# Kernel tuning notes

Hardware: AMD Instinct MI355X
Metric: run time of the kernel (lower is better)

The kernel has to match this reference:

```python
import jax, jax.numpy as jnp
import numpy as np

ND, NG, E = 25000, 20000, 1_000_000
DIN_D, DIN_G, H, OUT = 128, 128, 128, 128


def setup_inputs() -> dict:
    key = jax.random.key(0)
    ks = jax.random.split(key, 12)

    def w(k, i, o):
        return jax.random.normal(k, (i, o), jnp.float32) / np.float32(np.sqrt(i))

    return {
        "x_disease": jax.random.normal(ks[0], (ND, DIN_D), jnp.float32),
        "x_gene": jax.random.normal(ks[1], (NG, DIN_G), jnp.float32),
        "src": jax.random.randint(ks[2], (E,), 0, ND, dtype=jnp.int32),  # disease endpoint
        "dst": jax.random.randint(ks[3], (E,), 0, NG, dtype=jnp.int32),  # gene endpoint
        # layer 1, relation disease->gene: lin_l acts on aggregated disease feats, lin_r on gene feats
        "w1_dg_l": w(ks[4], DIN_D, H), "b1_dg": jnp.zeros((H,), jnp.float32), "w1_dg_r": w(ks[5], DIN_G, H),
        # layer 1, relation gene->disease (reverse edges)
        "w1_gd_l": w(ks[6], DIN_G, H), "b1_gd": jnp.zeros((H,), jnp.float32), "w1_gd_r": w(ks[7], DIN_D, H),
        # layer 2
        "w2_dg_l": w(ks[8], H, OUT), "b2_dg": jnp.zeros((OUT,), jnp.float32), "w2_dg_r": w(ks[9], H, OUT),
        "w2_gd_l": w(ks[10], H, OUT), "b2_gd": jnp.zeros((OUT,), jnp.float32), "w2_gd_r": w(ks[11], H, OUT),
    }


def _sage(x_src, x_dst, e_src, e_dst, n_dst, W_l, b_l, W_r):
    """Bipartite SAGEConv: lin_l(mean of source neighbors) + lin_r(x_dst)."""
    msg = x_src[e_src]                                         # [E, d] gather
    s = jax.ops.segment_sum(msg, e_dst, num_segments=n_dst)    # [n_dst, d]
    cnt = jax.ops.segment_sum(jnp.ones((e_dst.shape[0],), x_src.dtype),
                              e_dst, num_segments=n_dst)
    mean = s / jnp.maximum(cnt, 1.0)[:, None]                  # isolated nodes -> 0
    return mean @ W_l + b_l + x_dst @ W_r


def reference(x_disease, x_gene, src, dst,
              w1_dg_l, b1_dg, w1_dg_r, w1_gd_l, b1_gd, w1_gd_r,
              w2_dg_l, b2_dg, w2_dg_r, w2_gd_l, b2_gd, w2_gd_r):
    # HeteroConv aggr='sum': each node type receives from exactly one relation here,
    # so the cross-relation sum is the single relation output.
    g1 = _sage(x_disease, x_gene, src, dst, NG, w1_dg_l, b1_dg, w1_dg_r)   # gene <- disease
    d1 = _sage(x_gene, x_disease, dst, src, ND, w1_gd_l, b1_gd, w1_gd_r)   # disease <- gene (rev)
    g2 = _sage(d1, g1, src, dst, NG, w2_dg_l, b2_dg, w2_dg_r)
    d2 = _sage(g1, d1, dst, src, ND, w2_gd_l, b2_gd, w2_gd_r)
    return d2, g2
```

## Files before the change

kernel.cpp:

```cpp
#include <hip/hip_runtime.h>
#include <hip/hip_fp16.h>

#define ND 25000
#define NG 20000
#define NTOT (ND + NG)
#define NBLK 128
#define PREPB 1024
#define NSB 176
#define DRNG 6250
#define GRNG 5000
#define AGG_SLOTS 1563
#define AGG_GRID (8 * AGG_SLOTS)

typedef _Float16 half8 __attribute__((ext_vector_type(8)));
typedef float f32x4 __attribute__((ext_vector_type(4)));
typedef float f32x2 __attribute__((ext_vector_type(2)));

#define OFF_CNT    0ull
#define OFF_ROW    180224ull
#define OFF_PARTD  360704ull
#define OFF_PARTG  6760704ull
#define OFF_COL    11880704ull
#define OFF_WSW    15880704ull
#define OFF_XDH    16142848ull
#define OFF_XGH    22542848ull
#define OFF_X8D    27662848ull
#define OFF_X8G    30862848ull
#define OFF_MDH    33422848ull
#define OFF_MGH    39822848ull
#define OFF_D1H    44942848ull
#define OFF_G1H    51342848ull
#define OFF_D18    56462848ull
#define OFF_G18    59662848ull

struct WPtrs { const float* w[8]; };

__global__ __launch_bounds__(256) void prep_hist(const float* __restrict__ xd,
                                                 const float* __restrict__ xg,
                                                 __half* __restrict__ ydh,
                                                 __half* __restrict__ ygh,
                                                 unsigned char* __restrict__ y8d,
                                                 unsigned char* __restrict__ y8g,
                                                 WPtrs wp, _Float16* __restrict__ wsw,
                                                 const int* __restrict__ src,
                                                 const int* __restrict__ dst,
                                                 unsigned short* __restrict__ partD,
                                                 unsigned short* __restrict__ partG,
                                                 unsigned int* __restrict__ flags, int E) {
    __shared__ unsigned int h[12544];
    int bx = blockIdx.x, t = threadIdx.x;
    if (bx < 2 * NBLK) {
        bool isD = bx < NBLK;
        int bb = isD ? bx : bx - NBLK;
        const int* key = isD ? src : dst;
        int nw = isD ? (ND / 2) : (NG / 2);
        for (int i = t; i < nw; i += 256) h[i] = 0;
        __syncthreads();
        int e0 = (int)(((long long)E * bb) / NBLK);
        int e1 = (int)(((long long)E * (bb + 1)) / NBLK);
        for (int e = e0 + t; e < e1; e += 256) {
            int k = key[e];
            atomicAdd(&h[k >> 1], 1u << ((k & 1) * 16));
        }
        __syncthreads();
        unsigned int* po = (unsigned int*)((isD ? partD : partG) + (size_t)bb * (isD ? ND : NG));
        for (int i = t; i < nw; i += 256) po[i] = h[i];
        return;
    }
    int pb = bx - 2 * NBLK;
    if (pb < 8) {
        const float* W = wp.w[pb];
        _Float16* o = wsw + (size_t)pb * 16384;
        for (int rep = 0; rep < 8; ++rep) {
            int slot = rep * 256 + t;
            int lane = slot & 63, grp = slot >> 6;
            int kc = grp & 3, ntile = grp >> 2;
            int nn = ntile * 16 + (lane & 15);
            int kb = kc * 32 + (lane >> 4) * 8;
            half8 v;
#pragma unroll
            for (int j = 0; j < 8; ++j) v[j] = (_Float16)W[(size_t)(kb + j) * 128 + nn];
            *(half8*)(o + (size_t)slot * 8) = v;
        }
    } else if (pb == 8 && t < NSB) {
        flags[t] = 0u;
    }
    const int ndq = ND * 32;
    const int tot = ndq + NG * 32;
    for (int i = pb * 256 + t; i < tot; i += PREPB * 256) {
        const float* x;
        __half* y;
        unsigned char* y8;
        int idx;
        if (i < ndq) { x = xd; y = ydh; y8 = y8d; idx = i; }
        else         { x = xg; y = ygh; y8 = y8g; idx = i - ndq; }
        float4 v = ((const float4*)x)[idx];
        ((__half2*)y)[idx * 2 + 0] = __floats2half2_rn(v.x, v.y);
        ((__half2*)y)[idx * 2 + 1] = __floats2half2_rn(v.z, v.w);
        int p8 = __builtin_amdgcn_cvt_pk_fp8_f32(v.x, v.y, 0, false);
        p8 = __builtin_amdgcn_cvt_pk_fp8_f32(v.z, v.w, p8, true);
        ((int*)y8)[idx] = p8;
    }
}

__global__ __launch_bounds__(256) void scanall(unsigned short* __restrict__ partD,
                                               unsigned short* __restrict__ partG,
                                               int* __restrict__ row,
                                               unsigned int* __restrict__ flags, int E) {
    __shared__ int sd[256];
    __shared__ int sbase;
    int t = threadIdx.x, bid = blockIdx.x;
    int k = bid * 256 + t;
    int run = 0;
    if (k < NTOT) {
        unsigned short* part;
        int nb, kk;
        if (k < ND) { part = partD; nb = ND; kk = k; }
        else        { part = partG; nb = NG; kk = k - ND; }
#pragma unroll 8
        for (int b = 0; b < NBLK; ++b) {
            size_t idx = (size_t)b * nb + kk;
            int v = part[idx];
            part[idx] = (unsigned short)run;
            run += v;
        }
    }
    int tsum = run;
    sd[t] = tsum;
    __syncthreads();
    for (int off = 1; off < 256; off <<= 1) {
        int x = (t >= off) ? sd[t - off] : 0;
        __syncthreads();
        sd[t] += x;
        __syncthreads();
    }
    if (t == 0) {
        unsigned int agg = (unsigned int)sd[255] + 1u;
        __hip_atomic_store(&flags[bid], agg, __ATOMIC_RELEASE, __HIP_MEMORY_SCOPE_AGENT);
    }
    if (t < 64) {
        int s = 0;
        for (int i = t; i < bid; i += 64) {
            unsigned int v;
            do {
                v = __hip_atomic_load(&flags[i], __ATOMIC_ACQUIRE, __HIP_MEMORY_SCOPE_AGENT);
            } while (v == 0u);
            s += (int)v - 1;
        }
#pragma unroll
        for (int off = 1; off < 64; off <<= 1) s += __shfl_xor(s, off, 64);
        if (t == 0) sbase = s;
    }
    __syncthreads();
    int base = sbase;
    if (k < NTOT) row[k] = base + sd[t] - tsum;
    if (bid == 0 && t == 0) row[NTOT] = 2 * E;
}

__global__ __launch_bounds__(256) void fill2x(const int* __restrict__ src,
                                              const int* __restrict__ dst,
                                              const int* __restrict__ row,
                                              const unsigned short* __restrict__ partD,
                                              const unsigned short* __restrict__ partG,
                                              unsigned short* __restrict__ col, int E) {
    __shared__ unsigned int cur[DRNG];
    int t = threadIdx.x, bid = blockIdx.x;
    int x = bid & 7;
    int s = bid >> 3;
    bool isD = x < 4;
    int r0, rng, nbase, nb;
    const int *key, *val;
    const unsigned short* part;
    if (isD) { r0 = x * DRNG;       rng = DRNG; key = src; val = dst; part = partD; nb = ND; nbase = 0;  }
    else     { r0 = (x - 4) * GRNG; rng = GRNG; key = dst; val = src; part = partG; nb = NG; nbase = ND; }
    for (int i = t; i < rng; i += 256)
        cur[i] = (unsigned int)row[nbase + r0 + i] + part[(size_t)s * nb + r0 + i];
    __syncthreads();
    int e0 = (int)(((long long)E * s) / NBLK);
    int e1 = (int)(((long long)E * (s + 1)) / NBLK);
    for (int e = e0 + t; e < e1; e += 256) {
        int k = key[e];
        if (k >= r0 && k < r0 + rng) {
            unsigned int p = atomicAdd(&cur[k - r0], 1u);
            col[p] = (unsigned short)val[e];
        }
    }
}

__global__ __launch_bounds__(256, 8) void agg8m(const unsigned char* __restrict__ Xg,
                                                const unsigned char* __restrict__ Xd,
                                                const int* __restrict__ row,
                                                const unsigned short* __restrict__ col,
                                                __half* __restrict__ outd,
                                                __half* __restrict__ outg) {
    int wid = threadIdx.x >> 6, lane = threadIdx.x & 63;
    int bid = blockIdx.x;
    int xcd = bid & 7, slot = bid >> 3;
    const unsigned char* X;
    _Float16* out;
    int node, nloc;
    if (xcd < 4) {
        int loc = slot * 4 + wid;
        if (loc >= DRNG) return;
        nloc = xcd * DRNG + loc;
        if (nloc >= ND) return;
        node = nloc;
        X = Xg; out = (_Float16*)outd;
    } else {
        int loc = slot * 4 + wid;
        if (loc >= GRNG) return;
        nloc = (xcd - 4) * GRNG + loc;
        if (nloc >= NG) return;
        node = ND + nloc;
        X = Xd; out = (_Float16*)outg;
    }
    int b = row[node], e = row[node + 1];
    int g = lane >> 3, f = lane & 7;
    float acc[16];
#pragma unroll
    for (int k = 0; k < 16; ++k) acc[k] = 0.f;
    int j = b + g;
    for (; j + 8 < e; j += 16) {
        int c0 = col[j], c1 = col[j + 8];
        int4 w0 = *(const int4*)(X + (size_t)c0 * 128 + f * 16);
        int4 w1 = *(const int4*)(X + (size_t)c1 * 128 + f * 16);
        const int* wa = (const int*)&w0;
        const int* wb = (const int*)&w1;
#pragma unroll
        for (int q = 0; q < 4; ++q) {
            f32x2 l0 = __builtin_amdgcn_cvt_pk_f32_fp8(wa[q], false);
            f32x2 h0 = __builtin_amdgcn_cvt_pk_f32_fp8(wa[q], true);
            f32x2 l1 = __builtin_amdgcn_cvt_pk_f32_fp8(wb[q], false);
            f32x2 h1 = __builtin_amdgcn_cvt_pk_f32_fp8(wb[q], true);
            acc[q * 4 + 0] += l0[0] + l1[0];
            acc[q * 4 + 1] += l0[1] + l1[1];
            acc[q * 4 + 2] += h0[0] + h1[0];
            acc[q * 4 + 3] += h0[1] + h1[1];
        }
    }
    if (j < e) {
        int c = col[j];
        int4 w = *(const int4*)(X + (size_t)c * 128 + f * 16);
        const int* wa = (const int*)&w;
#pragma unroll
        for (int q = 0; q < 4; ++q) {
            f32x2 l = __builtin_amdgcn_cvt_pk_f32_fp8(wa[q], false);
            f32x2 h = __builtin_amdgcn_cvt_pk_f32_fp8(wa[q], true);
            acc[q * 4 + 0] += l[0];
            acc[q * 4 + 1] += l[1];
            acc[q * 4 + 2] += h[0];
            acc[q * 4 + 3] += h[1];
        }
    }
#pragma unroll
    for (int k = 0; k < 16; ++k) {
        acc[k] += __shfl_xor(acc[k], 8, 64);
        acc[k] += __shfl_xor(acc[k], 16, 64);
        acc[k] += __shfl_xor(acc[k], 32, 64);
    }
    if (g == 0) {
        int deg = e - b;
        float r = 1.0f / (float)(deg > 0 ? deg : 1);
        half8 o0, o1;
#pragma unroll
        for (int k = 0; k < 8; ++k) o0[k] = (_Float16)(acc[k] * r);
#pragma unroll
        for (int k = 0; k < 8; ++k) o1[k] = (_Float16)(acc[8 + k] * r);
        _Float16* op = out + (size_t)nloc * 128 + f * 16;
        *(half8*)op = o0;
        *(half8*)(op + 8) = o1;
    }
}

struct GemmDual {
    const __half *A1d, *A2d, *A1g, *A2g;
    const _Float16 *W1d, *W2d, *W1g, *W2g;
    const float *biasd, *biasg;
    float *Yfd, *Yfg;
    __half *Yhd, *Yhg;
    unsigned char *Y8d, *Y8g;
};
__global__ __launch_bounds__(256) void gemm2(GemmDual p, int nblkD, int layer) {
    int bx = blockIdx.x;
    bool isD = bx < nblkD;
    const __half* A1 = isD ? p.A1d : p.A1g;
    const __half* A2 = isD ? p.A2d : p.A2g;
    const _Float16* W1 = isD ? p.W1d : p.W1g;
    const _Float16* W2 = isD ? p.W2d : p.W2g;
    const float* bias = isD ? p.biasd : p.biasg;
    float* Yf = isD ? p.Yfd : p.Yfg;
    __half* Yh = isD ? p.Yhd : p.Yhg;
    unsigned char* Y8 = isD ? p.Y8d : p.Y8g;
    int n = isD ? ND : NG, b0 = isD ? bx : bx - nblkD;
    int t = threadIdx.x;
    int wave = t >> 6, lane = t & 63;
    int row0 = b0 * 64 + wave * 16;
    if (row0 >= n) return;
    int m = lane & 15, quad = lane >> 4;
    int arow = row0 + m;
    if (arow >= n) arow = n - 1;
    const _Float16* a1p = (const _Float16*)A1 + (size_t)arow * 128 + quad * 8;
    const _Float16* a2p = (const _Float16*)A2 + (size_t)arow * 128 + quad * 8;
    half8 a1[4], a2[4];
#pragma unroll
    for (int kc = 0; kc < 4; ++kc) {
        a1[kc] = *(const half8*)(a1p + kc * 32);
        a2[kc] = *(const half8*)(a2p + kc * 32);
    }
#pragma unroll
    for (int ntile = 0; ntile < 8; ++ntile) {
        f32x4 acc = {0.f, 0.f, 0.f, 0.f};
#pragma unroll
        for (int kc = 0; kc < 4; ++kc) {
            half8 b1 = *(const half8*)(W1 + (size_t)((ntile * 4 + kc) * 64 + lane) * 8);
            acc = __builtin_amdgcn_mfma_f32_16x16x32_f16(a1[kc], b1, acc, 0, 0, 0);
            half8 b2 = *(const half8*)(W2 + (size_t)((ntile * 4 + kc) * 64 + lane) * 8);
            acc = __builtin_amdgcn_mfma_f32_16x16x32_f16(a2[kc], b2, acc, 0, 0, 0);
        }
        int colx = ntile * 16 + m;
        float bb = bias[colx];
#pragma unroll
        for (int r = 0; r < 4; ++r) {
            int rr = row0 + quad * 4 + r;
            if (rr < n) {
                float v = acc[r] + bb;
                if (layer == 2) {
                    Yf[(size_t)rr * 128 + colx] = v;
                } else {
                    Yh[(size_t)rr * 128 + colx] = __float2half(v);
                    int p8 = __builtin_amdgcn_cvt_pk_fp8_f32(v, v, 0, false);
                    Y8[(size_t)rr * 128 + colx] = (unsigned char)(p8 & 0xff);
                }
            }
        }
    }
}

extern "C" void kernel_launch(void* const* d_in, const int* in_sizes, int n_in,
                              void* d_out, int out_size, void* d_ws, size_t ws_size,
                              hipStream_t stream) {
    const float* x_d = (const float*)d_in[0];
    const float* x_g = (const float*)d_in[1];
    const int*   src = (const int*)d_in[2];
    const int*   dst = (const int*)d_in[3];
    float* out = (float*)d_out;

    char* ws = (char*)d_ws;
    unsigned int*   flags = (unsigned int*)(ws + OFF_CNT);
    int*            row   = (int*)(ws + OFF_ROW);
    unsigned short* partD = (unsigned short*)(ws + OFF_PARTD);
    unsigned short* partG = (unsigned short*)(ws + OFF_PARTG);
    unsigned short* col   = (unsigned short*)(ws + OFF_COL);
    _Float16*       wsw   = (_Float16*)(ws + OFF_WSW);
    __half*         xd_h  = (__half*)(ws + OFF_XDH);
    __half*         xg_h  = (__half*)(ws + OFF_XGH);
    unsigned char*  x8d   = (unsigned char*)(ws + OFF_X8D);
    unsigned char*  x8g   = (unsigned char*)(ws + OFF_X8G);
    __half*         md_h  = (__half*)(ws + OFF_MDH);
    __half*         mg_h  = (__half*)(ws + OFF_MGH);
    __half*         d1_h  = (__half*)(ws + OFF_D1H);
    __half*         g1_h  = (__half*)(ws + OFF_G1H);
    unsigned char*  d1_8  = (unsigned char*)(ws + OFF_D18);
    unsigned char*  g1_8  = (unsigned char*)(ws + OFF_G18);

    const int E = in_sizes[2];
    const int nblkD = (ND + 63) / 64;
    const int nblkG = (NG + 63) / 64;

    WPtrs wp;
    wp.w[0] = (const float*)d_in[4];
    wp.w[1] = (const float*)d_in[6];
    wp.w[2] = (const float*)d_in[7];
    wp.w[3] = (const float*)d_in[9];
    wp.w[4] = (const float*)d_in[10];
    wp.w[5] = (const float*)d_in[12];
    wp.w[6] = (const float*)d_in[13];
    wp.w[7] = (const float*)d_in[15];
    const float* b1_dg = (const float*)d_in[5];
    const float* b1_gd = (const float*)d_in[8];
    const float* b2_dg = (const float*)d_in[11];
    const float* b2_gd = (const float*)d_in[14];

    prep_hist<<<2 * NBLK + PREPB, 256, 0, stream>>>(x_d, x_g, xd_h, xg_h, x8d, x8g,
                                                    wp, wsw, src, dst, partD, partG, flags, E);
    scanall<<<NSB, 256, 0, stream>>>(partD, partG, row, flags, E);
    fill2x<<<NBLK * 8, 256, 0, stream>>>(src, dst, row, partD, partG, col, E);

    agg8m<<<AGG_GRID, 256, 0, stream>>>(x8g, x8d, row, col, md_h, mg_h);
    GemmDual g1p;
    g1p.A1d = md_h; g1p.A2d = xd_h; g1p.W1d = wsw + 2 * 16384; g1p.W2d = wsw + 3 * 16384;
    g1p.biasd = b1_gd; g1p.Yfd = nullptr; g1p.Yhd = d1_h; g1p.Y8d = d1_8;
    g1p.A1g = mg_h; g1p.A2g = xg_h; g1p.W1g = wsw + 0 * 16384; g1p.W2g = wsw + 1 * 16384;
    g1p.biasg = b1_dg; g1p.Yfg = nullptr; g1p.Yhg = g1_h; g1p.Y8g = g1_8;
    gemm2<<<nblkD + nblkG, 256, 0, stream>>>(g1p, nblkD, 1);

    agg8m<<<AGG_GRID, 256, 0, stream>>>(g1_8, d1_8, row, col, md_h, mg_h);
    GemmDual g2p;
    g2p.A1d = md_h; g2p.A2d = d1_h; g2p.W1d = wsw + 6 * 16384; g2p.W2d = wsw + 7 * 16384;
    g2p.biasd = b2_gd; g2p.Yfd = out; g2p.Yhd = nullptr; g2p.Y8d = nullptr;
    g2p.A1g = mg_h; g2p.A2g = g1_h; g2p.W1g = wsw + 4 * 16384; g2p.W2g = wsw + 5 * 16384;
    g2p.biasg = b2_dg; g2p.Yfg = out + (size_t)ND * 128; g2p.Yhg = nullptr; g2p.Y8g = nullptr;
    gemm2<<<nblkD + nblkG, 256, 0, stream>>>(g2p, nblkD, 2);
}
```

Before: 253.4 us.

## Fuse scan and CSR fill into one kernel with grid barrier; unroll aggregation x4

Merges the prefix-scan and column-fill kernels into a single launch. The first NSB blocks do the scan and then bump a global counter, and every block spins on that counter before filling. This saves one kernel launch and the gap between launches, but it relies on the scan blocks staying resident while the other blocks spin. Separately, the fp8 neighbor aggregation loop now handles four edges per iteration instead of two to put more gathers in flight, and the tail becomes a loop.

```diff
diff --git a/kernel.cpp b/kernel.cpp
--- a/kernel.cpp
+++ b/kernel.cpp
@@ -7,6 +7,7 @@
 #define NBLK 128
 #define PREPB 1024
 #define NSB 176
+#define SFB 1024
 #define DRNG 6250
 #define GRNG 5000
 #define AGG_SLOTS 1563
@@ -82,7 +83,7 @@
             for (int j = 0; j < 8; ++j) v[j] = (_Float16)W[(size_t)(kb + j) * 128 + nn];
             *(half8*)(o + (size_t)slot * 8) = v;
         }
-    } else if (pb == 8 && t < NSB) {
+    } else if (pb == 8 && t <= NSB) {
         flags[t] = 0u;
     }
     const int ndq = ND * 32;
@@ -103,68 +104,72 @@
     }
 }
 
-__global__ __launch_bounds__(256) void scanall(unsigned short* __restrict__ partD,
-                                               unsigned short* __restrict__ partG,
-                                               int* __restrict__ row,
-                                               unsigned int* __restrict__ flags, int E) {
-    __shared__ int sd[256];
+__global__ __launch_bounds__(256) void scanfill(unsigned short* __restrict__ partD,
+                                                unsigned short* __restrict__ partG,
+                                                int* __restrict__ row,
+                                                unsigned int* __restrict__ flags,
+                                                const int* __restrict__ src,
+                                                const int* __restrict__ dst,
+                                                unsigned short* __restrict__ col, int E) {
+    __shared__ unsigned int cur[DRNG];
     __shared__ int sbase;
     int t = threadIdx.x, bid = blockIdx.x;
-    int k = bid * 256 + t;
-    int run = 0;
-    if (k < NTOT) {
-        unsigned short* part;
-        int nb, kk;
-        if (k < ND) { part = partD; nb = ND; kk = k; }
-        else        { part = partG; nb = NG; kk = k - ND; }
+    int* sd = (int*)cur;
+    if (bid < NSB) {
+        int k = bid * 256 + t;
+        int run = 0;
+        if (k < NTOT) {
+            unsigned short* part;
+            int nb, kk;
+            if (k < ND) { part = partD; nb = ND; kk = k; }
+            else        { part = partG; nb = NG; kk = k - ND; }
 #pragma unroll 8
-        for (int b = 0; b < NBLK; ++b) {
-            size_t idx = (size_t)b * nb + kk;
-            int v = part[idx];
-            part[idx] = (unsigned short)run;
-            run += v;
-        }
-    }
-    int tsum = run;
-    sd[t] = tsum;
+            for (int b = 0; b < NBLK; ++b) {
+                size_t idx = (size_t)b * nb + kk;
+                int v = part[idx];
+                part[idx] = (unsigned short)run;
+                run += v;
+            }
+        }
+        int tsum = run;
+        sd[t] = tsum;
+        __syncthreads();
+        for (int off = 1; off < 256; off <<= 1) {
+            int x = (t >= off) ? sd[t - off] : 0;
+            __syncthreads();
+            sd[t] += x;
+            __syncthreads();
+        }
+        if (t == 0)
+            __hip_atomic_store(&flags[bid], (unsigned int)sd[255] + 1u,
+                               __ATOMIC_RELEASE, __HIP_MEMORY_SCOPE_AGENT);
+        if (t < 64) {
+            int s = 0;
+            for (int i = t; i < bid; i += 64) {
+                unsigned int v;
+                do {
+                    v = __hip_atomic_load(&flags[i], __ATOMIC_ACQUIRE, __HIP_MEMORY_SCOPE_AGENT);
+                } while (v == 0u);
+                s += (int)v - 1;
+            }
+#pragma unroll
+            for (int off = 1; off < 64; off <<= 1) s += __shfl_xor(s, off, 64);
+            if (t == 0) sbase = s;
+        }
+        __syncthreads();
+        if (k < NTOT) row[k] = sbase + sd[t] - tsum;
+        if (bid == 0 && t == 0) row[NTOT] = 2 * E;
+        __syncthreads();
+        if (t == 0)
+            __hip_atomic_fetch_add((int*)&flags[NSB], 1,
+                                   __ATOMIC_RELEASE, __HIP_MEMORY_SCOPE_AGENT);
+    }
+    if (t == 0) {
+        while (__hip_atomic_load((int*)&flags[NSB], __ATOMIC_ACQUIRE,
+                                 __HIP_MEMORY_SCOPE_AGENT) < NSB)
+            __builtin_amdgcn_s_sleep(2);
+    }
     __syncthreads();
-    for (int off = 1; off < 256; off <<= 1) {
-        int x = (t >= off) ? sd[t - off] : 0;
-        __syncthreads();
-        sd[t] += x;
-        __syncthreads();
-    }
-    if (t == 0) {
-        unsigned int agg = (unsigned int)sd[255] + 1u;
-        __hip_atomic_store(&flags[bid], agg, __ATOMIC_RELEASE, __HIP_MEMORY_SCOPE_AGENT);
-    }
-    if (t < 64) {
-        int s = 0;
-        for (int i = t; i < bid; i += 64) {
-            unsigned int v;
-            do {
-                v = __hip_atomic_load(&flags[i], __ATOMIC_ACQUIRE, __HIP_MEMORY_SCOPE_AGENT);
-            } while (v == 0u);
-            s += (int)v - 1;
-        }
-#pragma unroll
-        for (int off = 1; off < 64; off <<= 1) s += __shfl_xor(s, off, 64);
-        if (t == 0) sbase = s;
-    }
-    __syncthreads();
-    int base = sbase;
-    if (k < NTOT) row[k] = base + sd[t] - tsum;
-    if (bid == 0 && t == 0) row[NTOT] = 2 * E;
-}
-
-__global__ __launch_bounds__(256) void fill2x(const int* __restrict__ src,
-                                              const int* __restrict__ dst,
-                                              const int* __restrict__ row,
-                                              const unsigned short* __restrict__ partD,
-                                              const unsigned short* __restrict__ partG,
-                                              unsigned short* __restrict__ col, int E) {
-    __shared__ unsigned int cur[DRNG];
-    int t = threadIdx.x, bid = blockIdx.x;
     int x = bid & 7;
     int s = bid >> 3;
     bool isD = x < 4;
@@ -220,25 +225,33 @@
 #pragma unroll
     for (int k = 0; k < 16; ++k) acc[k] = 0.f;
     int j = b + g;
-    for (; j + 8 < e; j += 16) {
-        int c0 = col[j], c1 = col[j + 8];
+    for (; j + 24 < e; j += 32) {
+        int c0 = col[j], c1 = col[j + 8], c2 = col[j + 16], c3 = col[j + 24];
         int4 w0 = *(const int4*)(X + (size_t)c0 * 128 + f * 16);
         int4 w1 = *(const int4*)(X + (size_t)c1 * 128 + f * 16);
+        int4 w2 = *(const int4*)(X + (size_t)c2 * 128 + f * 16);
+        int4 w3 = *(const int4*)(X + (size_t)c3 * 128 + f * 16);
         const int* wa = (const int*)&w0;
         const int* wb = (const int*)&w1;
+        const int* wc = (const int*)&w2;
+        const int* wd = (const int*)&w3;
 #pragma unroll
         for (int q = 0; q < 4; ++q) {
             f32x2 l0 = __builtin_amdgcn_cvt_pk_f32_fp8(wa[q], false);
             f32x2 h0 = __builtin_amdgcn_cvt_pk_f32_fp8(wa[q], true);
             f32x2 l1 = __builtin_amdgcn_cvt_pk_f32_fp8(wb[q], false);
             f32x2 h1 = __builtin_amdgcn_cvt_pk_f32_fp8(wb[q], true);
-            acc[q * 4 + 0] += l0[0] + l1[0];
-            acc[q * 4 + 1] += l0[1] + l1[1];
-            acc[q * 4 + 2] += h0[0] + h1[0];
-            acc[q * 4 + 3] += h0[1] + h1[1];
-        }
-    }
-    if (j < e) {
+            f32x2 l2 = __builtin_amdgcn_cvt_pk_f32_fp8(wc[q], false);
+            f32x2 h2 = __builtin_amdgcn_cvt_pk_f32_fp8(wc[q], true);
+            f32x2 l3 = __builtin_amdgcn_cvt_pk_f32_fp8(wd[q], false);
+            f32x2 h3 = __builtin_amdgcn_cvt_pk_f32_fp8(wd[q], true);
+            acc[q * 4 + 0] += (l0[0] + l1[0]) + (l2[0] + l3[0]);
+            acc[q * 4 + 1] += (l0[1] + l1[1]) + (l2[1] + l3[1]);
+            acc[q * 4 + 2] += (h0[0] + h1[0]) + (h2[0] + h3[0]);
+            acc[q * 4 + 3] += (h0[1] + h1[1]) + (h2[1] + h3[1]);
+        }
+    }
+    for (; j < e; j += 8) {
         int c = col[j];
         int4 w = *(const int4*)(X + (size_t)c * 128 + f * 16);
         const int* wa = (const int*)&w;
@@ -383,8 +396,7 @@
 
     prep_hist<<<2 * NBLK + PREPB, 256, 0, stream>>>(x_d, x_g, xd_h, xg_h, x8d, x8g,
                                                     wp, wsw, src, dst, partD, partG, flags, E);
-    scanall<<<NSB, 256, 0, stream>>>(partD, partG, row, flags, E);
-    fill2x<<<NBLK * 8, 256, 0, stream>>>(src, dst, row, partD, partG, col, E);
+    scanfill<<<SFB, 256, 0, stream>>>(partD, partG, row, flags, src, dst, col, E);
 
     agg8m<<<AGG_GRID, 256, 0, stream>>>(x8g, x8d, row, col, md_h, mg_h);
     GemmDual g1p;
```

After: 412.7 us. 1.63x slower.
